# Optimization experiments

Hardware: AMD Instinct MI355X
Metric: run time of the kernel (lower is better)

## Reference

```python
import jax, jax.numpy as jnp
import numpy as np

THRESHOLD = 0.4
TOPK = 4


def _box_iou(boxes1, boxes2):
    # boxes1: [B, Q, 4], boxes2: [B, G, 4] in (x1, y1, x2, y2)
    area1 = (boxes1[..., 2] - boxes1[..., 0]) * (boxes1[..., 3] - boxes1[..., 1])  # [B,Q]
    area2 = (boxes2[..., 2] - boxes2[..., 0]) * (boxes2[..., 3] - boxes2[..., 1])  # [B,G]
    lt = jnp.maximum(boxes1[:, :, None, :2], boxes2[:, None, :, :2])  # [B,Q,G,2]
    rb = jnp.minimum(boxes1[:, :, None, 2:], boxes2[:, None, :, 2:])  # [B,Q,G,2]
    wh = jnp.clip(rb - lt, 0.0)
    inter = wh[..., 0] * wh[..., 1]                                   # [B,Q,G]
    union = area1[:, :, None] + area2[:, None, :] - inter
    return inter / (union + 1e-07)


def _make_boxes(key, b, n):
    k1, k2 = jax.random.split(key)
    xy = jax.random.uniform(k1, (b, n, 2), dtype=jnp.float32) * 0.8
    wh = jax.random.uniform(k2, (b, n, 2), dtype=jnp.float32) * 0.2 + 0.01
    return jnp.concatenate([xy, xy + wh], axis=-1)  # valid x1<x2, y1<y2


def setup_inputs() -> dict:
    key = jax.random.key(0)
    k1, k2, k3 = jax.random.split(key, 3)
    B, Q, G = 128, 1000, 300
    pred_logits = jax.random.normal(k1, (B, Q, 1), dtype=jnp.float32)
    pred_boxes_xyxy = _make_boxes(k2, B, Q)
    tgt_boxes_xyxy = _make_boxes(k3, B, G)
    return {
        "pred_logits": pred_logits,
        "pred_boxes_xyxy": pred_boxes_xyxy,
        "tgt_boxes_xyxy": tgt_boxes_xyxy,
    }


def reference(pred_logits, pred_boxes_xyxy, tgt_boxes_xyxy):
    # Per-query binary score.
    score = jax.nn.sigmoid(pred_logits)[..., 0]              # [B,Q]
    iou = _box_iou(pred_boxes_xyxy, tgt_boxes_xyxy)          # [B,Q,G]
    valid = (iou > THRESHOLD).astype(score.dtype)
    gt_score = score[:, :, None] * iou * valid               # [B,Q,G]
    # Per-GT top-k over queries (same matches as the nested-loop original:
    # invalid entries are zero, and positives-only are kept via the mask).
    vals, idxs = jax.lax.top_k(jnp.swapaxes(gt_score, 1, 2), TOPK)  # [B,G,K]
    mask = vals > 0.0                                        # valid match mask
    return vals, idxs.astype(jnp.int32), mask
```

## Files before the change

### kernel.cpp

```cpp
#include <hip/hip_runtime.h>

#define NB 128
#define NQ 1000
#define NG 300
#define NK 4
#define THRESH 0.4f

#define GCHUNKS  6
#define GPERB    50
#define NTHREADS 256
#define QPT      4
#define QCAP     24
#define CAP      48

__global__ __launch_bounds__(NTHREADS) void fused_matcher(
    const float* __restrict__ logits,
    const float* __restrict__ pboxes,
    const float* __restrict__ tboxes,
    float* __restrict__ out_vals,
    float* __restrict__ out_idx,
    float* __restrict__ out_mask)
{
    __shared__ float4 stb[GPERB + 1];
    __shared__ unsigned scnt[GPERB];
    __shared__ unsigned short sslot[GPERB][CAP];
    __shared__ unsigned short queue[QCAP][NTHREADS];

    const int b   = blockIdx.y;
    const int gc  = blockIdx.x;
    const int tid = threadIdx.x;
    const int g0  = gc * GPERB;

    const float4* __restrict__ tb4 =
        reinterpret_cast<const float4*>(tboxes) + (size_t)b * NG + g0;
    const float4* __restrict__ pb4 =
        reinterpret_cast<const float4*>(pboxes) + (size_t)b * NQ;

    if (tid < GPERB) {
        stb[tid]  = tb4[tid];
        scnt[tid] = 0u;
    }
    if (tid == 0) stb[GPERB] = make_float4(2e9f, 2e9f, 2e9f, 2e9f);

    const float4 dummy = make_float4(2e9f, 2e9f, 2e9f, 2e9f);
    float4 pA = pb4[tid];
    float4 pB = pb4[NTHREADS + tid];
    float4 pC = pb4[2 * NTHREADS + tid];
    float4 pD = (3 * NTHREADS + tid < NQ) ? pb4[3 * NTHREADS + tid] : dummy;
    const float aA = 0.999f * ((pA.z - pA.x) * (pA.w - pA.y));
    const float aB = 0.999f * ((pB.z - pB.x) * (pB.w - pB.y));
    const float aC = 0.999f * ((pC.z - pC.x) * (pC.w - pC.y));
    const float aD = 0.999f * ((pD.z - pD.x) * (pD.w - pD.y));

    __syncthreads();

    int cnt = 0;
    float4 tc = stb[0];
#define TEST(P, A, SEL)                                                     \
    {                                                                       \
        float ltx = fmaxf(P.x, tc.x);                                       \
        float lty = fmaxf(P.y, tc.y);                                       \
        float rbx = fminf(P.z, tc.z);                                       \
        float rby = fminf(P.w, tc.w);                                       \
        float w = fmaxf(rbx - ltx, 0.0f);                                   \
        float h = fmaxf(rby - lty, 0.0f);                                   \
        float inter = w * h;                                                \
        bool pass = fmaf(inter, 3.5f, -(A)) >= ta999;                       \
        if (pass && cnt < QCAP)                                             \
            queue[cnt][tid] = (unsigned short)((gi << 2) | (SEL));          \
        cnt += pass ? 1 : 0;                                                \
    }
    for (int gi = 0; gi < GPERB; ++gi) {
        float4 tn = stb[gi + 1];
        const float ta999 = 0.999f * ((tc.z - tc.x) * (tc.w - tc.y));
        TEST(pA, aA, 0)
        TEST(pB, aB, 1)
        TEST(pC, aC, 2)
        TEST(pD, aD, 3)
        tc = tn;
    }
#undef TEST

    const int m = cnt < QCAP ? cnt : QCAP;
    for (int i = 0; i < m; ++i) {
        const int e   = queue[i][tid];
        const int gi  = e >> 2;
        const int q   = (e & 3) * NTHREADS + tid;
        unsigned pos = atomicAdd(&scnt[gi], 1u);
        if (pos < CAP) sslot[gi][pos] = (unsigned short)q;
    }
    __syncthreads();

    const int grp = tid >> 2;
    const int l4  = tid & 3;
    if (grp < GPERB) {
        const float4 tb = stb[grp];
        const float tarea = (tb.z - tb.x) * (tb.w - tb.y);
        int n = (int)scnt[grp];
        if (n > CAP) n = CAP;
        const float* __restrict__ lg = logits + (size_t)b * NQ;

        unsigned long long k0 = 0ull, k1 = 0ull, k2 = 0ull, k3 = 0ull;
        for (int i = l4; i < n; i += 4) {
            const int q = sslot[grp][i];
            const float4 pp = pb4[q];
            float parea = (pp.z - pp.x) * (pp.w - pp.y);
            float ltx = fmaxf(pp.x, tb.x);
            float lty = fmaxf(pp.y, tb.y);
            float rbx = fminf(pp.z, tb.z);
            float rby = fminf(pp.w, tb.w);
            float w = fmaxf(rbx - ltx, 0.0f);
            float h = fmaxf(rby - lty, 0.0f);
            float inter = w * h;
            float uni   = parea + tarea - inter;
            float iou   = inter / (uni + 1e-7f);
            if (iou > THRESH) {
                float x   = lg[q];
                float sc  = 1.0f / (1.0f + expf(-x));
                float val = sc * iou;
                unsigned long long ck =
                    ((unsigned long long)__float_as_uint(val) << 32) |
                    (unsigned long long)(unsigned)(~(unsigned)q);
                if (ck > k3) {
                    if (ck > k0)      { k3 = k2; k2 = k1; k1 = k0; k0 = ck; }
                    else if (ck > k1) { k3 = k2; k2 = k1; k1 = ck; }
                    else if (ck > k2) { k3 = k2; k2 = ck; }
                    else              { k3 = ck; }
                }
            }
        }

#define MERGE_STEP(MASK)                                                    \
        {                                                                   \
            unsigned long long p0 = __shfl_xor(k0, MASK, 64);               \
            unsigned long long p1 = __shfl_xor(k1, MASK, 64);               \
            unsigned long long p2 = __shfl_xor(k2, MASK, 64);               \
            unsigned long long p3 = __shfl_xor(k3, MASK, 64);               \
            k0 = k0 > p3 ? k0 : p3;                                         \
            k1 = k1 > p2 ? k1 : p2;                                         \
            k2 = k2 > p1 ? k2 : p1;                                         \
            k3 = k3 > p0 ? k3 : p0;                                         \
            unsigned long long t;                                           \
            if (k0 < k2) { t = k0; k0 = k2; k2 = t; }                       \
            if (k1 < k3) { t = k1; k1 = k3; k3 = t; }                       \
            if (k0 < k1) { t = k0; k0 = k1; k1 = t; }                       \
            if (k2 < k3) { t = k2; k2 = k3; k3 = t; }                       \
        }
        MERGE_STEP(1)
        MERGE_STEP(2)
#undef MERGE_STEP

        if (l4 == 0) {
            const int iq0 = k0 ? (int)~(unsigned)k0 : -1;
            const int iq1 = k1 ? (int)~(unsigned)k1 : -1;
            const int iq2 = k2 ? (int)~(unsigned)k2 : -1;
            float4 vv, vi, vm;
            float* pv = &vv.x; float* pi_ = &vi.x; float* pm = &vm.x;
            int fill = 0;
#define EMIT(J, KJ)                                                         \
            {                                                               \
                if (KJ != 0ull) {                                           \
                    pv[J]  = __uint_as_float((unsigned)(KJ >> 32));         \
                    pi_[J] = (float)(int)~(unsigned)KJ;                     \
                    pm[J]  = 1.0f;                                          \
                } else {                                                    \
                    while (fill == iq0 || fill == iq1 || fill == iq2)       \
                        ++fill;                                             \
                    pv[J]  = 0.0f;                                          \
                    pi_[J] = (float)fill;                                   \
                    pm[J]  = 0.0f;                                          \
                    ++fill;                                                 \
                }                                                           \
            }
            EMIT(0, k0) EMIT(1, k1) EMIT(2, k2) EMIT(3, k3)
#undef EMIT
            const size_t o4 = (size_t)b * NG + g0 + grp;
            reinterpret_cast<float4*>(out_vals)[o4] = vv;
            reinterpret_cast<float4*>(out_idx)[o4]  = vi;
            reinterpret_cast<float4*>(out_mask)[o4] = vm;
        }
    }
}

extern "C" void kernel_launch(void* const* d_in, const int* in_sizes, int n_in,
                              void* d_out, int out_size, void* d_ws, size_t ws_size,
                              hipStream_t stream) {
    const float* logits = (const float*)d_in[0];
    const float* pboxes = (const float*)d_in[1];
    const float* tboxes = (const float*)d_in[2];

    float* out = (float*)d_out;
    const size_t bgk = (size_t)NB * NG * NK;
    float* out_vals = out;
    float* out_idx  = out + bgk;
    float* out_mask = out + 2 * bgk;

    dim3 grid(GCHUNKS, NB);
    fused_matcher<<<grid, NTHREADS, 0, stream>>>(logits, pboxes, tboxes,
                                                 out_vals, out_idx, out_mask);
}
```

Before: 33.27 us.

## Replace shared-memory candidate queue with per-thread bitmasks, halve GT chunk size

Each thread now records its prefilter hits as 25-bit register masks, one per query slot, and drains them with ffs into the per-GT slot lists. This replaces the 12KB shared-memory queue and its store/reload traffic. The GT chunk is halved to 25 so the mask fits in 32 bits, which doubles the grid to 12 chunks per batch. Each block still reloads all 1000 predicted boxes, so that work doubles, and only 100 of 256 threads do the top-k phase.

Result: slower. 35.01 us (+5.2%).

```diff
diff --git a/kernel.cpp b/kernel.cpp
--- a/kernel.cpp
+++ b/kernel.cpp
@@ -6,11 +6,9 @@
 #define NK 4
 #define THRESH 0.4f
 
-#define GCHUNKS  6
-#define GPERB    50
+#define GCHUNKS  12
+#define GPERB    25
 #define NTHREADS 256
-#define QPT      4
-#define QCAP     24
 #define CAP      48
 
 __global__ __launch_bounds__(NTHREADS) void fused_matcher(
@@ -24,7 +22,6 @@
     __shared__ float4 stb[GPERB + 1];
     __shared__ unsigned scnt[GPERB];
     __shared__ unsigned short sslot[GPERB][CAP];
-    __shared__ unsigned short queue[QCAP][NTHREADS];
 
     const int b   = blockIdx.y;
     const int gc  = blockIdx.x;
@@ -40,7 +37,7 @@
         stb[tid]  = tb4[tid];
         scnt[tid] = 0u;
     }
-    if (tid == 0) stb[GPERB] = make_float4(2e9f, 2e9f, 2e9f, 2e9f);
+    if (tid == GPERB) stb[GPERB] = make_float4(2e9f, 2e9f, 2e9f, 2e9f);
 
     const float4 dummy = make_float4(2e9f, 2e9f, 2e9f, 2e9f);
     float4 pA = pb4[tid];
@@ -54,9 +51,9 @@
 
     __syncthreads();
 
-    int cnt = 0;
+    unsigned mA = 0u, mB = 0u, mC = 0u, mD = 0u;
     float4 tc = stb[0];
-#define TEST(P, A, SEL)                                                     \
+#define TEST(P, A, M)                                                       \
     {                                                                       \
         float ltx = fmaxf(P.x, tc.x);                                       \
         float lty = fmaxf(P.y, tc.y);                                       \
@@ -65,30 +62,32 @@
         float w = fmaxf(rbx - ltx, 0.0f);                                   \
         float h = fmaxf(rby - lty, 0.0f);                                   \
         float inter = w * h;                                                \
-        bool pass = fmaf(inter, 3.5f, -(A)) >= ta999;                       \
-        if (pass && cnt < QCAP)                                             \
-            queue[cnt][tid] = (unsigned short)((gi << 2) | (SEL));          \
-        cnt += pass ? 1 : 0;                                                \
-    }
+        unsigned pass = (fmaf(inter, 3.5f, -(A)) >= ta999) ? 1u : 0u;       \
+        M = (M << 1) | pass;                                                \
+    }
+#pragma unroll
     for (int gi = 0; gi < GPERB; ++gi) {
         float4 tn = stb[gi + 1];
         const float ta999 = 0.999f * ((tc.z - tc.x) * (tc.w - tc.y));
-        TEST(pA, aA, 0)
-        TEST(pB, aB, 1)
-        TEST(pC, aC, 2)
-        TEST(pD, aD, 3)
+        TEST(pA, aA, mA)
+        TEST(pB, aB, mB)
+        TEST(pC, aC, mC)
+        TEST(pD, aD, mD)
         tc = tn;
     }
 #undef TEST
 
-    const int m = cnt < QCAP ? cnt : QCAP;
-    for (int i = 0; i < m; ++i) {
-        const int e   = queue[i][tid];
-        const int gi  = e >> 2;
-        const int q   = (e & 3) * NTHREADS + tid;
-        unsigned pos = atomicAdd(&scnt[gi], 1u);
-        if (pos < CAP) sslot[gi][pos] = (unsigned short)q;
-    }
+#define DRAIN(M, SLOT)                                                      \
+    while (M) {                                                             \
+        int p  = __ffs(M) - 1;                                              \
+        M &= M - 1u;                                                        \
+        int gi = (GPERB - 1) - p;                                           \
+        unsigned pos = atomicAdd(&scnt[gi], 1u);                            \
+        if (pos < CAP)                                                      \
+            sslot[gi][pos] = (unsigned short)((SLOT)*NTHREADS + tid);       \
+    }
+    DRAIN(mA, 0) DRAIN(mB, 1) DRAIN(mC, 2) DRAIN(mD, 3)
+#undef DRAIN
     __syncthreads();
 
     const int grp = tid >> 2;
```
